# Kernel tuning notes

Measured on AMD Instinct MI355X. Metric: run time of the kernel, lower is better.

Reference implementation:

```python
import jax, jax.numpy as jnp
import numpy as np


def setup_inputs() -> dict:
    key = jax.random.key(0)
    k1, k2 = jax.random.split(key)
    decoder_hidden = jax.random.normal(k1, (16, 1024, 1024), dtype=jnp.float32)
    encoder_outputs = jax.random.normal(k2, (16, 2048, 1024), dtype=jnp.float32)
    return {"decoder_hidden": decoder_hidden, "encoder_outputs": encoder_outputs}


def reference(decoder_hidden, encoder_outputs):
    # scores: [B, Q, K] = decoder_hidden @ encoder_outputs^T (no scaling, per source)
    scores = jnp.einsum('bqd,bkd->bqk', decoder_hidden, encoder_outputs)
    attn = jax.nn.softmax(scores, axis=-1)
    # context: [B, Q, D]
    context = jnp.einsum('bqk,bkd->bqd', attn, encoder_outputs)
    return (context, attn)
```

## Files before the change

### kernel.cpp

```cpp
#include <hip/hip_runtime.h>


typedef __attribute__((ext_vector_type(8))) short s8v;
typedef __attribute__((ext_vector_type(4))) float f32x4;
typedef __attribute__((ext_vector_type(8))) unsigned short us8;
typedef __attribute__((ext_vector_type(4))) unsigned short us4;

__device__ inline unsigned short f2bf(float f) {
    unsigned u = __builtin_bit_cast(unsigned, f);
    u += 0x7FFFu + ((u >> 16) & 1u);
    return (unsigned short)(u >> 16);
}
__device__ inline float bf2f(unsigned short h) {
    return __builtin_bit_cast(float, (unsigned)h << 16);
}

__device__ __forceinline__ s8v lds_read128(unsigned addr) {
    s8v d;
    asm volatile("ds_read_b128 %0, %1" : "=v"(d) : "v"(addr));
    return d;
}

__global__ __launch_bounds__(256)
void split_convert(const float* __restrict__ x, unsigned short* __restrict__ hi,
                   unsigned short* __restrict__ lo, int n4)
{
    int i = blockIdx.x * 256 + threadIdx.x;
    const int stride = gridDim.x * 256;
    for (; i < n4; i += stride) {
        const float4 v = reinterpret_cast<const float4*>(x)[i];
        us4 h, l;
        h.x = f2bf(v.x); l.x = f2bf(v.x - bf2f(h.x));
        h.y = f2bf(v.y); l.y = f2bf(v.y - bf2f(h.y));
        h.z = f2bf(v.z); l.z = f2bf(v.z - bf2f(h.z));
        h.w = f2bf(v.w); l.w = f2bf(v.w - bf2f(h.w));
        reinterpret_cast<us4*>(hi)[i] = h;
        reinterpret_cast<us4*>(lo)[i] = l;
    }
}

__global__ __launch_bounds__(256)
void transpose_bf16(const unsigned short* __restrict__ in, unsigned short* __restrict__ out)
{
    __shared__ unsigned short S[64][72];
    const int b  = blockIdx.z;
    const int kt = blockIdx.x;
    const int dt = blockIdx.y;
    const unsigned short* ib = in  + (size_t)b * 2048 * 1024 + (size_t)kt * 64 * 1024 + (size_t)dt * 64;
    unsigned short*       ob = out + (size_t)b * 1024 * 2048 + (size_t)dt * 64 * 2048 + (size_t)kt * 64;

    const int tid = threadIdx.x;
    const int r0 = tid >> 3, c8 = (tid & 7) * 8;
    #pragma unroll
    for (int p = 0; p < 2; ++p) {
        const int r = r0 + 32 * p;
        const us8 v = *reinterpret_cast<const us8*>(&ib[(size_t)r * 1024 + c8]);
        *reinterpret_cast<us8*>(&S[r][c8]) = v;
    }
    __syncthreads();
    const int d0 = tid >> 3, k8 = (tid & 7) * 8;
    #pragma unroll
    for (int p = 0; p < 2; ++p) {
        const int d = d0 + 32 * p;
        us8 w;
        #pragma unroll
        for (int j = 0; j < 8; ++j) w[j] = S[k8 + j][d];
        *reinterpret_cast<us8*>(&ob[(size_t)d * 2048 + k8]) = w;
    }
}

template<int NPASS, int KPP, int NXT, int NYT>
__global__ __launch_bounds__(512, 2)
void gemm_nt_256(const unsigned short* __restrict__ A0,
                 const unsigned short* __restrict__ A1,
                 const unsigned short* __restrict__ A2,
                 const unsigned short* __restrict__ B0,
                 const unsigned short* __restrict__ B1,
                 const unsigned short* __restrict__ B2,
                 float* __restrict__ Out,
                 const int ldA, const int ldB, const int ldO,
                 const long long sA, const long long sB, const long long sO)
{
    constexpr int TPP = KPP / 32;
    constexpr int NT  = NPASS * TPP;
    extern __shared__ unsigned short smem[];

    int flat = blockIdx.x + NXT * (blockIdx.y + NYT * (int)blockIdx.z);
    const int nwg = NXT * NYT * (int)gridDim.z;
    flat = (flat & 7) * (nwg >> 3) + (flat >> 3);
    const int nt = flat % NXT;
    const int mt = (flat / NXT) % NYT;
    const int b  = flat / (NXT * NYT);

    const int tid = threadIdx.x, lane = tid & 63, wid = tid >> 6;
    const int wm = wid >> 2, wn = wid & 3;

    const size_t arow = (size_t)b * sA + (size_t)(mt * 256) * ldA;
    const size_t brow = (size_t)b * sB + (size_t)(nt * 256) * ldB;
    const unsigned short* Ap0 = A0 + arow;
    const unsigned short* Ap1 = A1 + arow;
    const unsigned short* Ap2 = A2 + arow;
    const unsigned short* Bp0 = B0 + brow;
    const unsigned short* Bp1 = B1 + brow;
    const unsigned short* Bp2 = B2 + brow;

    const int ci0 = tid, ci1 = 512 + tid;
    const int r0 = ci0 >> 2, r1 = ci1 >> 2;
    const int cs0 = ((ci0 & 3) ^ ((r0 >> 1) & 3)) * 8;
    const int cs1 = ((ci1 & 3) ^ ((r1 >> 1) & 3)) * 8;
    const int aoff0 = r0 * ldA + cs0, aoff1 = r1 * ldA + cs1;
    const int boff0 = r0 * ldB + cs0, boff1 = r1 * ldB + cs1;
    const int wd0 = wid * 512;
    const int wd1 = 4096 + wid * 512;

    auto stageA = [&](int t) {
        const int p  = t / TPP;
        const int k0 = (t % TPP) * 32;
        const unsigned short* As = (p == 0) ? Ap0 : (p == 1 ? Ap1 : Ap2);
        unsigned short* d = smem + (t & 3) * 16384;
        __builtin_amdgcn_global_load_lds(
            (const __attribute__((address_space(1))) void*)(As + k0 + aoff0),
            (__attribute__((address_space(3))) void*)(d + wd0), 16, 0, 0);
        __builtin_amdgcn_global_load_lds(
            (const __attribute__((address_space(1))) void*)(As + k0 + aoff1),
            (__attribute__((address_space(3))) void*)(d + wd1), 16, 0, 0);
    };
    auto stageB = [&](int t) {
        const int p  = t / TPP;
        const int k0 = (t % TPP) * 32;
        const unsigned short* Bs = (p == 0) ? Bp0 : (p == 1 ? Bp1 : Bp2);
        unsigned short* d = smem + (t & 3) * 16384 + 8192;
        __builtin_amdgcn_global_load_lds(
            (const __attribute__((address_space(1))) void*)(Bs + k0 + boff0),
            (__attribute__((address_space(3))) void*)(d + wd0), 16, 0, 0);
        __builtin_amdgcn_global_load_lds(
            (const __attribute__((address_space(1))) void*)(Bs + k0 + boff1),
            (__attribute__((address_space(3))) void*)(d + wd1), 16, 0, 0);
    };

    const int fr = lane & 15;
    const int kc = lane >> 4;
    unsigned offA[8], offB[4];
    #pragma unroll
    for (int m = 0; m < 8; ++m) {
        const int R = wm * 128 + m * 16 + fr;
        offA[m] = (unsigned)(R * 64) + ((unsigned)(kc ^ ((R >> 1) & 3)) << 4);
    }
    #pragma unroll
    for (int n = 0; n < 4; ++n) {
        const int R = wn * 64 + n * 16 + fr;
        offB[n] = 16384u + (unsigned)(R * 64) + ((unsigned)(kc ^ ((R >> 1) & 3)) << 4);
    }

    const unsigned lds0 =
        (unsigned)(uintptr_t)(__attribute__((address_space(3))) unsigned short*)smem;

    f32x4 acc[8][4];
    #pragma unroll
    for (int m = 0; m < 8; ++m)
        #pragma unroll
        for (int n = 0; n < 4; ++n) acc[m][n] = (f32x4){0.f, 0.f, 0.f, 0.f};

    stageA(0); stageB(0); stageA(1); stageB(1); stageA(2); stageB(2);
    asm volatile("s_waitcnt vmcnt(4)" ::: "memory");
    __builtin_amdgcn_s_barrier();

    s8v fA[8], fB[4], gA[8], gB[4];
    #pragma unroll
    for (int n = 0; n < 4; ++n) fB[n] = lds_read128(lds0 + offB[n]);
    #pragma unroll
    for (int m = 0; m < 8; ++m) fA[m] = lds_read128(lds0 + offA[m]);

    auto tile_body = [&](const int t, s8v (&ca)[8], s8v (&cb)[4],
                         s8v (&na)[8], s8v (&nb)[4]) {
        if (t + 3 < NT) { stageA(t + 3); stageB(t + 3); }
        if (t + 1 < NT) {
            const unsigned nbase = lds0 + (unsigned)((t + 1) & 3) * 32768u;
            #pragma unroll
            for (int n = 0; n < 4; ++n) nb[n] = lds_read128(nbase + offB[n]);
            #pragma unroll
            for (int m = 0; m < 8; ++m) na[m] = lds_read128(nbase + offA[m]);
            asm volatile("s_waitcnt lgkmcnt(12)" ::: "memory");
        } else {
            asm volatile("s_waitcnt lgkmcnt(0)" ::: "memory");
        }
        __builtin_amdgcn_sched_barrier(0);
        __builtin_amdgcn_s_setprio(1);
        #pragma unroll
        for (int m = 0; m < 8; ++m)
            #pragma unroll
            for (int n = 0; n < 4; ++n)
                acc[m][n] = __builtin_amdgcn_mfma_f32_16x16x32_bf16(ca[m], cb[n], acc[m][n], 0, 0, 0);
        __builtin_amdgcn_s_setprio(0);
        if (t + 3 < NT)      asm volatile("s_waitcnt vmcnt(4)" ::: "memory");
        else if (t + 2 < NT) asm volatile("s_waitcnt vmcnt(0)" ::: "memory");
        __builtin_amdgcn_s_barrier();
    };

    for (int tt = 0; tt < NT; tt += 2) {
        tile_body(tt,     fA, fB, gA, gB);
        tile_body(tt + 1, gA, gB, fA, fB);
    }

    float* Ob = Out + (size_t)b * sO + (size_t)(mt * 256 + wm * 128) * ldO + nt * 256 + wn * 64;
    const int cr = (lane >> 4) << 2;
    const int cc = lane & 15;
    #pragma unroll
    for (int m = 0; m < 8; ++m)
        #pragma unroll
        for (int n = 0; n < 4; ++n)
            #pragma unroll
            for (int r = 0; r < 4; ++r)
                Ob[(size_t)(m * 16 + cr + r) * ldO + n * 16 + cc] = acc[m][n][r];
}

__global__ __launch_bounds__(256)
void softmax_rows_bf(float* __restrict__ P, unsigned short* __restrict__ Pb)
{
    float* p = P + (size_t)blockIdx.x * 2048;
    unsigned short* pb = Pb + (size_t)blockIdx.x * 2048;
    const int tid = threadIdx.x;

    float4 v0 = *reinterpret_cast<const float4*>(&p[tid * 4]);
    float4 v1 = *reinterpret_cast<const float4*>(&p[1024 + tid * 4]);

    float m = fmaxf(fmaxf(fmaxf(v0.x, v0.y), fmaxf(v0.z, v0.w)),
                    fmaxf(fmaxf(v1.x, v1.y), fmaxf(v1.z, v1.w)));
    #pragma unroll
    for (int off = 32; off; off >>= 1) m = fmaxf(m, __shfl_xor(m, off));

    __shared__ float red[8];
    const int wid = tid >> 6;
    if ((tid & 63) == 0) red[wid] = m;
    __syncthreads();
    m = fmaxf(fmaxf(red[0], red[1]), fmaxf(red[2], red[3]));

    v0.x = __expf(v0.x - m); v0.y = __expf(v0.y - m);
    v0.z = __expf(v0.z - m); v0.w = __expf(v0.w - m);
    v1.x = __expf(v1.x - m); v1.y = __expf(v1.y - m);
    v1.z = __expf(v1.z - m); v1.w = __expf(v1.w - m);

    float s = ((v0.x + v0.y) + (v0.z + v0.w)) + ((v1.x + v1.y) + (v1.z + v1.w));
    #pragma unroll
    for (int off = 32; off; off >>= 1) s += __shfl_xor(s, off);
    if ((tid & 63) == 0) red[4 + wid] = s;
    __syncthreads();
    const float inv = 1.0f / ((red[4] + red[5]) + (red[6] + red[7]));

    v0.x *= inv; v0.y *= inv; v0.z *= inv; v0.w *= inv;
    v1.x *= inv; v1.y *= inv; v1.z *= inv; v1.w *= inv;
    *reinterpret_cast<float4*>(&p[tid * 4]) = v0;
    *reinterpret_cast<float4*>(&p[1024 + tid * 4]) = v1;

    us4 h0, h1;
    h0.x = f2bf(v0.x); h0.y = f2bf(v0.y); h0.z = f2bf(v0.z); h0.w = f2bf(v0.w);
    h1.x = f2bf(v1.x); h1.y = f2bf(v1.y); h1.z = f2bf(v1.z); h1.w = f2bf(v1.w);
    *reinterpret_cast<us4*>(&pb[tid * 4]) = h0;
    *reinterpret_cast<us4*>(&pb[1024 + tid * 4]) = h1;
}

#define BM 128
#define BN 128
#define BK 32
#define LDT 132

template <bool TRANSB>
__global__ __launch_bounds__(256, 2)
void gemm_tile(const float* __restrict__ X, const float* __restrict__ Y,
               float* __restrict__ Out,
               int ldX, int ldY, int ldO, int KD,
               long long strideX, long long strideY, long long strideO)
{
    __shared__ float As[BK][LDT];
    __shared__ float Bs[BK][LDT];
    const int b  = blockIdx.z;
    const int mt = blockIdx.y;
    const int nt = blockIdx.x;
    const float* Xb = X + (size_t)b * strideX + (size_t)mt * BM * ldX;
    const float* Yb = TRANSB ? (Y + (size_t)b * strideY + (size_t)nt * BN * ldY)
                             : (Y + (size_t)b * strideY + (size_t)nt * BN);
    float* Ob = Out + (size_t)b * strideO + (size_t)mt * BM * ldO + (size_t)nt * BN;
    const int tid = threadIdx.x;
    const int tx = tid & 15;
    const int ty = tid >> 4;
    const int sr = tid >> 3;
    const int sc = (tid & 7) << 2;
    const int br = tid >> 5;
    const int bc = (tid & 31) << 2;
    float acc[8][8];
    #pragma unroll
    for (int i = 0; i < 8; ++i)
        #pragma unroll
        for (int j = 0; j < 8; ++j) acc[i][j] = 0.f;
    for (int k0 = 0; k0 < KD; k0 += BK) {
        #pragma unroll
        for (int p = 0; p < 4; ++p) {
            const float4 v = *reinterpret_cast<const float4*>(
                &Xb[(size_t)(sr + 32 * p) * ldX + k0 + sc]);
            As[sc + 0][sr + 32 * p] = v.x;
            As[sc + 1][sr + 32 * p] = v.y;
            As[sc + 2][sr + 32 * p] = v.z;
            As[sc + 3][sr + 32 * p] = v.w;
        }
        if (TRANSB) {
            #pragma unroll
            for (int p = 0; p < 4; ++p) {
                const float4 v = *reinterpret_cast<const float4*>(
                    &Yb[(size_t)(sr + 32 * p) * ldY + k0 + sc]);
                Bs[sc + 0][sr + 32 * p] = v.x;
                Bs[sc + 1][sr + 32 * p] = v.y;
                Bs[sc + 2][sr + 32 * p] = v.z;
                Bs[sc + 3][sr + 32 * p] = v.w;
            }
        } else {
            #pragma unroll
            for (int p = 0; p < 4; ++p) {
                const float4 v = *reinterpret_cast<const float4*>(
                    &Yb[(size_t)(k0 + br + 8 * p) * ldY + bc]);
                *reinterpret_cast<float4*>(&Bs[br + 8 * p][bc]) = v;
            }
        }
        __syncthreads();
        #pragma unroll 8
        for (int kk = 0; kk < BK; ++kk) {
            const float4 a0 = *reinterpret_cast<const float4*>(&As[kk][ty * 4]);
            const float4 a1 = *reinterpret_cast<const float4*>(&As[kk][64 + ty * 4]);
            const float4 b0 = *reinterpret_cast<const float4*>(&Bs[kk][tx * 4]);
            const float4 b1 = *reinterpret_cast<const float4*>(&Bs[kk][64 + tx * 4]);
            const float av[8] = {a0.x, a0.y, a0.z, a0.w, a1.x, a1.y, a1.z, a1.w};
            const float bv[8] = {b0.x, b0.y, b0.z, b0.w, b1.x, b1.y, b1.z, b1.w};
            #pragma unroll
            for (int i = 0; i < 8; ++i)
                #pragma unroll
                for (int j = 0; j < 8; ++j)
                    acc[i][j] = fmaf(av[i], bv[j], acc[i][j]);
        }
        __syncthreads();
    }
    #pragma unroll
    for (int i = 0; i < 8; ++i) {
        const int r = (i < 4) ? (ty * 4 + i) : (64 + ty * 4 + (i - 4));
        const float4 w0 = make_float4(acc[i][0], acc[i][1], acc[i][2], acc[i][3]);
        const float4 w1 = make_float4(acc[i][4], acc[i][5], acc[i][6], acc[i][7]);
        *reinterpret_cast<float4*>(&Ob[(size_t)r * ldO + tx * 4])      = w0;
        *reinterpret_cast<float4*>(&Ob[(size_t)r * ldO + 64 + tx * 4]) = w1;
    }
}

__global__ __launch_bounds__(256)
void softmax_rows(float* __restrict__ P)
{
    float* p = P + (size_t)blockIdx.x * 2048;
    const int tid = threadIdx.x;
    float4 v0 = *reinterpret_cast<const float4*>(&p[tid * 4]);
    float4 v1 = *reinterpret_cast<const float4*>(&p[1024 + tid * 4]);
    float m = fmaxf(fmaxf(fmaxf(v0.x, v0.y), fmaxf(v0.z, v0.w)),
                    fmaxf(fmaxf(v1.x, v1.y), fmaxf(v1.z, v1.w)));
    #pragma unroll
    for (int off = 32; off; off >>= 1) m = fmaxf(m, __shfl_xor(m, off));
    __shared__ float red[8];
    const int wid = tid >> 6;
    if ((tid & 63) == 0) red[wid] = m;
    __syncthreads();
    m = fmaxf(fmaxf(red[0], red[1]), fmaxf(red[2], red[3]));
    v0.x = __expf(v0.x - m); v0.y = __expf(v0.y - m);
    v0.z = __expf(v0.z - m); v0.w = __expf(v0.w - m);
    v1.x = __expf(v1.x - m); v1.y = __expf(v1.y - m);
    v1.z = __expf(v1.z - m); v1.w = __expf(v1.w - m);
    float s = ((v0.x + v0.y) + (v0.z + v0.w)) + ((v1.x + v1.y) + (v1.z + v1.w));
    #pragma unroll
    for (int off = 32; off; off >>= 1) s += __shfl_xor(s, off);
    if ((tid & 63) == 0) red[4 + wid] = s;
    __syncthreads();
    const float inv = 1.0f / ((red[4] + red[5]) + (red[6] + red[7]));
    v0.x *= inv; v0.y *= inv; v0.z *= inv; v0.w *= inv;
    v1.x *= inv; v1.y *= inv; v1.z *= inv; v1.w *= inv;
    *reinterpret_cast<float4*>(&p[tid * 4]) = v0;
    *reinterpret_cast<float4*>(&p[1024 + tid * 4]) = v1;
}

extern "C" void kernel_launch(void* const* d_in, const int* in_sizes, int n_in,
                              void* d_out, int out_size, void* d_ws, size_t ws_size,
                              hipStream_t stream)
{
    const float* dec = (const float*)d_in[0];
    const float* enc = (const float*)d_in[1];
    float* ctx  = (float*)d_out;
    float* attn = ctx + (size_t)16 * 1024 * 1024;

    const long long DECN = 16LL * 1024 * 1024;
    const long long ENCN = 16LL * 2048 * 1024;
    const size_t NEED = (size_t)(2 * DECN + 4 * ENCN) * 2;

    if (ws_size >= NEED) {
        unsigned short* decH  = (unsigned short*)d_ws;
        unsigned short* decL  = decH + DECN;
        unsigned short* encH  = decL + DECN;
        unsigned short* encL  = encH + ENCN;
        unsigned short* encT  = encL + ENCN;
        unsigned short* attnB = encT + ENCN;

        hipFuncSetAttribute((const void*)&gemm_nt_256<3, 1024, 8, 4>,
                            hipFuncAttributeMaxDynamicSharedMemorySize, 131072);
        hipFuncSetAttribute((const void*)&gemm_nt_256<1, 2048, 4, 4>,
                            hipFuncAttributeMaxDynamicSharedMemorySize, 131072);

        split_convert<<<2048, 256, 0, stream>>>(dec, decH, decL, (int)(DECN / 4));
        split_convert<<<2048, 256, 0, stream>>>(enc, encH, encL, (int)(ENCN / 4));
        transpose_bf16<<<dim3(32, 16, 16), 256, 0, stream>>>(encH, encT);

        gemm_nt_256<3, 1024, 8, 4><<<dim3(8, 4, 16), 512, 131072, stream>>>(
            decH, decH, decL, encH, encL, encH, attn,
            1024, 1024, 2048,
            1024LL * 1024, 2048LL * 1024, 1024LL * 2048);

        softmax_rows_bf<<<16 * 1024, 256, 0, stream>>>(attn, attnB);

        gemm_nt_256<1, 2048, 4, 4><<<dim3(4, 4, 16), 512, 131072, stream>>>(
            attnB, attnB, attnB, encT, encT, encT, ctx,
            2048, 2048, 1024,
            1024LL * 2048, 1024LL * 2048, 1024LL * 1024);
    } else {
        gemm_tile<true><<<dim3(2048 / BN, 1024 / BM, 16), 256, 0, stream>>>(
            dec, enc, attn, 1024, 1024, 2048, 1024,
            1024LL * 1024, 2048LL * 1024, 1024LL * 2048);
        softmax_rows<<<dim3(16 * 1024), 256, 0, stream>>>(attn);
        gemm_tile<false><<<dim3(1024 / BN, 1024 / BM, 16), 256, 0, stream>>>(
            attn, enc, ctx, 2048, 1024, 1024, 2048,
            1024LL * 2048, 2048LL * 1024, 1024LL * 1024);
    }
}
```

Baseline: 427.5 us.

## Fuse encoder split-convert with transpose and interleave LDS reads with MFMA groups

The encoder fp32 split into bf16 hi/lo and the transpose of the hi part now happen in one kernel. This saves a launch and a full re-read of encH. Inside the GEMM main loop, the next tile's LDS fragment reads are split into four chunks, each interleaved with a quarter of the MFMA work, using staged lgkmcnt waits. The global prefetch moves to the middle of the tile. The goal is to hide LDS latency behind matrix math rather than issuing all reads up front, at the cost of more complex waitcnt bookkeeping and some risk of wrong counts.

```diff
diff --git a/kernel.cpp b/kernel.cpp
--- a/kernel.cpp
+++ b/kernel.cpp
@@ -40,33 +40,55 @@
 }
 
 __global__ __launch_bounds__(256)
-void transpose_bf16(const unsigned short* __restrict__ in, unsigned short* __restrict__ out)
+void split_convert_enc(const float* __restrict__ enc,
+                       unsigned short* __restrict__ encH,
+                       unsigned short* __restrict__ encL,
+                       unsigned short* __restrict__ encT)
 {
     __shared__ unsigned short S[64][72];
     const int b  = blockIdx.z;
     const int kt = blockIdx.x;
     const int dt = blockIdx.y;
-    const unsigned short* ib = in  + (size_t)b * 2048 * 1024 + (size_t)kt * 64 * 1024 + (size_t)dt * 64;
-    unsigned short*       ob = out + (size_t)b * 1024 * 2048 + (size_t)dt * 64 * 2048 + (size_t)kt * 64;
-
     const int tid = threadIdx.x;
-    const int r0 = tid >> 3, c8 = (tid & 7) * 8;
-    #pragma unroll
-    for (int p = 0; p < 2; ++p) {
-        const int r = r0 + 32 * p;
-        const us8 v = *reinterpret_cast<const us8*>(&ib[(size_t)r * 1024 + c8]);
-        *reinterpret_cast<us8*>(&S[r][c8]) = v;
-    }
+
+    const int r   = tid >> 2;
+    const int c16 = (tid & 3) * 16;
+
+    const size_t inoff = (size_t)b * 2048 * 1024 + (size_t)(kt * 64 + r) * 1024 + dt * 64 + c16;
+    const float4* src = reinterpret_cast<const float4*>(enc + inoff);
+
+    us8 h0, h1, l0, l1;
+    #pragma unroll
+    for (int q = 0; q < 2; ++q) {
+        const float4 a = src[q * 2 + 0];
+        const float4 c = src[q * 2 + 1];
+        us8& h = q ? h1 : h0;
+        us8& l = q ? l1 : l0;
+        h[0] = f2bf(a.x); l[0] = f2bf(a.x - bf2f(h[0]));
+        h[1] = f2bf(a.y); l[1] = f2bf(a.y - bf2f(h[1]));
+        h[2] = f2bf(a.z); l[2] = f2bf(a.z - bf2f(h[2]));
+        h[3] = f2bf(a.w); l[3] = f2bf(a.w - bf2f(h[3]));
+        h[4] = f2bf(c.x); l[4] = f2bf(c.x - bf2f(h[4]));
+        h[5] = f2bf(c.y); l[5] = f2bf(c.y - bf2f(h[5]));
+        h[6] = f2bf(c.z); l[6] = f2bf(c.z - bf2f(h[6]));
+        h[7] = f2bf(c.w); l[7] = f2bf(c.w - bf2f(h[7]));
+    }
+    *reinterpret_cast<us8*>(&encH[inoff])     = h0;
+    *reinterpret_cast<us8*>(&encH[inoff + 8]) = h1;
+    *reinterpret_cast<us8*>(&encL[inoff])     = l0;
+    *reinterpret_cast<us8*>(&encL[inoff + 8]) = l1;
+    *reinterpret_cast<us8*>(&S[r][c16])     = h0;
+    *reinterpret_cast<us8*>(&S[r][c16 + 8]) = h1;
     __syncthreads();
-    const int d0 = tid >> 3, k8 = (tid & 7) * 8;
-    #pragma unroll
-    for (int p = 0; p < 2; ++p) {
-        const int d = d0 + 32 * p;
-        us8 w;
-        #pragma unroll
-        for (int j = 0; j < 8; ++j) w[j] = S[k8 + j][d];
-        *reinterpret_cast<us8*>(&ob[(size_t)d * 2048 + k8]) = w;
-    }
+
+    const int d   = tid >> 2;
+    const int k16 = (tid & 3) * 16;
+    us8 w0, w1;
+    #pragma unroll
+    for (int j = 0; j < 8; ++j) { w0[j] = S[k16 + j][d]; w1[j] = S[k16 + 8 + j][d]; }
+    const size_t outoff = (size_t)b * 1024 * 2048 + (size_t)(dt * 64 + d) * 2048 + kt * 64 + k16;
+    *reinterpret_cast<us8*>(&encT[outoff])     = w0;
+    *reinterpret_cast<us8*>(&encT[outoff + 8]) = w1;
 }
 
 template<int NPASS, int KPP, int NXT, int NYT>
@@ -172,35 +194,84 @@
     for (int m = 0; m < 8; ++m) fA[m] = lds_read128(lds0 + offA[m]);
 
     auto tile_body = [&](const int t, s8v (&ca)[8], s8v (&cb)[4],
-                         s8v (&na)[8], s8v (&nb)[4]) {
+                         s8v (&na)[8], s8v (&nb)[4], const bool reads) {
+        const unsigned nbase = lds0 + (unsigned)((t + 1) & 3) * 32768u;
+        __builtin_amdgcn_s_setprio(1);
+
+        if (reads) {
+            nb[0] = lds_read128(nbase + offB[0]);
+            nb[1] = lds_read128(nbase + offB[1]);
+            nb[2] = lds_read128(nbase + offB[2]);
+            nb[3] = lds_read128(nbase + offB[3]);
+            na[0] = lds_read128(nbase + offA[0]);
+            na[1] = lds_read128(nbase + offA[1]);
+            asm volatile("s_waitcnt lgkmcnt(12)" ::: "memory");
+        } else {
+            asm volatile("s_waitcnt lgkmcnt(6)" ::: "memory");
+        }
+        __builtin_amdgcn_sched_barrier(0);
+        #pragma unroll
+        for (int m = 0; m < 2; ++m)
+            #pragma unroll
+            for (int n = 0; n < 4; ++n)
+                acc[m][n] = __builtin_amdgcn_mfma_f32_16x16x32_bf16(ca[m], cb[n], acc[m][n], 0, 0, 0);
+
+        if (reads) {
+            na[2] = lds_read128(nbase + offA[2]);
+            na[3] = lds_read128(nbase + offA[3]);
+            asm volatile("s_waitcnt lgkmcnt(12)" ::: "memory");
+        } else {
+            asm volatile("s_waitcnt lgkmcnt(4)" ::: "memory");
+        }
+        __builtin_amdgcn_sched_barrier(0);
+        #pragma unroll
+        for (int m = 2; m < 4; ++m)
+            #pragma unroll
+            for (int n = 0; n < 4; ++n)
+                acc[m][n] = __builtin_amdgcn_mfma_f32_16x16x32_bf16(ca[m], cb[n], acc[m][n], 0, 0, 0);
+
         if (t + 3 < NT) { stageA(t + 3); stageB(t + 3); }
-        if (t + 1 < NT) {
-            const unsigned nbase = lds0 + (unsigned)((t + 1) & 3) * 32768u;
-            #pragma unroll
-            for (int n = 0; n < 4; ++n) nb[n] = lds_read128(nbase + offB[n]);
-            #pragma unroll
-            for (int m = 0; m < 8; ++m) na[m] = lds_read128(nbase + offA[m]);
+
+        if (reads) {
+            na[4] = lds_read128(nbase + offA[4]);
+            na[5] = lds_read128(nbase + offA[5]);
+            asm volatile("s_waitcnt lgkmcnt(12)" ::: "memory");
+        } else {
+            asm volatile("s_waitcnt lgkmcnt(2)" ::: "memory");
+        }
+        __builtin_amdgcn_sched_barrier(0);
+        #pragma unroll
+        for (int m = 4; m < 6; ++m)
+            #pragma unroll
+            for (int n = 0; n < 4; ++n)
+                acc[m][n] = __builtin_amdgcn_mfma_f32_16x16x32_bf16(ca[m], cb[n], acc[m][n], 0, 0, 0);
+
+        if (reads) {
+            na[6] = lds_read128(nbase + offA[6]);
+            na[7] = lds_read128(nbase + offA[7]);
             asm volatile("s_waitcnt lgkmcnt(12)" ::: "memory");
         } else {
             asm volatile("s_waitcnt lgkmcnt(0)" ::: "memory");
         }
         __builtin_amdgcn_sched_barrier(0);
-        __builtin_amdgcn_s_setprio(1);
-        #pragma unroll
-        for (int m = 0; m < 8; ++m)
+        #pragma unroll
+        for (int m = 6; m < 8; ++m)
             #pragma unroll
             for (int n = 0; n < 4; ++n)
                 acc[m][n] = __builtin_amdgcn_mfma_f32_16x16x32_bf16(ca[m], cb[n], acc[m][n], 0, 0, 0);
         __builtin_amdgcn_s_setprio(0);
+
         if (t + 3 < NT)      asm volatile("s_waitcnt vmcnt(4)" ::: "memory");
         else if (t + 2 < NT) asm volatile("s_waitcnt vmcnt(0)" ::: "memory");
         __builtin_amdgcn_s_barrier();
     };
 
-    for (int tt = 0; tt < NT; tt += 2) {
-        tile_body(tt,     fA, fB, gA, gB);
-        tile_body(tt + 1, gA, gB, fA, fB);
-    }
+    for (int tt = 0; tt < NT - 2; tt += 2) {
+        tile_body(tt,     fA, fB, gA, gB, true);
+        tile_body(tt + 1, gA, gB, fA, fB, true);
+    }
+    tile_body(NT - 2, fA, fB, gA, gB, true);
+    tile_body(NT - 1, gA, gB, fA, fB, false);
 
     float* Ob = Out + (size_t)b * sO + (size_t)(mt * 256 + wm * 128) * ldO + nt * 256 + wn * 64;
     const int cr = (lane >> 4) << 2;
@@ -406,8 +477,7 @@
                             hipFuncAttributeMaxDynamicSharedMemorySize, 131072);
 
         split_convert<<<2048, 256, 0, stream>>>(dec, decH, decL, (int)(DECN / 4));
-        split_convert<<<2048, 256, 0, stream>>>(enc, encH, encL, (int)(ENCN / 4));
-        transpose_bf16<<<dim3(32, 16, 16), 256, 0, stream>>>(encH, encT);
+        split_convert_enc<<<dim3(32, 16, 16), 256, 0, stream>>>(enc, encH, encL, encT);
 
         gemm_nt_256<3, 1024, 8, 4><<<dim3(8, 4, 16), 512, 131072, stream>>>(
             decH, decH, decL, encH, encL, encH, attn,
```

New measurement: 422.9 us. About the same (-1.1%).
